# Kernel optimization log

Hardware: AMD Instinct MI355X
Metric: run time of the kernel (lower is better)

## Reference

```python
import jax, jax.numpy as jnp
import numpy as np

B, L, H = 2, 4096, 1024
ED, N, R, K = 2048, 16, 64, 4


def setup_inputs() -> dict:
    key = jax.random.key(0)
    ks = jax.random.split(key, 8)
    w = lambda i, shape, s=0.02: jax.random.normal(ks[i], shape, jnp.float32) * s
    # dt bias initialized like Mamba: inv-softplus of dt ~ logU(1e-3, 1e-1)
    dt = jnp.exp(jax.random.uniform(ks[7], (ED,)) * (np.log(0.1) - np.log(0.001)) + np.log(0.001))
    dt = jnp.clip(dt, 1e-4)
    inv_dt = dt + jnp.log(-jnp.expm1(-dt))
    A = jnp.broadcast_to(jnp.arange(1, N + 1, dtype=jnp.float32), (ED, N))
    return dict(
        x=jax.random.normal(ks[0], (B, L, H), jnp.float32),
        in_proj_w=w(1, (2 * ED, H)),
        conv_w=w(2, (ED, K), 0.2),
        conv_b=jnp.zeros((ED,), jnp.float32),
        x_proj_w=w(3, (R + 2 * N, ED)),
        dt_w=w(4, (ED, R), 64 ** -0.5),
        dt_b=inv_dt,
        A_log=jnp.log(A),
        D=jnp.ones((ED,), jnp.float32),
        out_proj_w=w(5, (H, ED)),
    )


def reference(x, in_proj_w, conv_w, conv_b, x_proj_w, dt_w, dt_b, A_log, D, out_proj_w):
    Bq, Lq, Hq = x.shape
    EDq, Kq = conv_w.shape
    Rq = dt_w.shape[1]
    Nq = A_log.shape[1]

    # in_proj -> [B, L, 2*ED]; chunk into hidden_states and gate
    xz = jnp.einsum('blh,eh->ble', x, in_proj_w)
    hs, gate = jnp.split(xz, 2, axis=-1)

    # causal depthwise conv1d along L (padding K-1 on the left), then SiLU
    hs_pad = jnp.pad(hs, ((0, 0), (Kq - 1, 0), (0, 0)))  # [B, L+K-1, ED]
    conv = conv_b
    for k in range(Kq):  # K=4, fixed small loop
        conv = conv + hs_pad[:, k:k + Lq, :] * conv_w[:, k]
    hs = jax.nn.silu(conv)  # [B, L, ED]

    # x_proj -> split into dt (rank R), B (N), C (N)
    ssm = jnp.einsum('ble,pe->blp', hs, x_proj_w)
    dtr, Bm, Cm = jnp.split(ssm, [Rq, Rq + Nq], axis=-1)

    # dt_proj + softplus (delta_softplus=True with delta_bias)
    delta = jax.nn.softplus(jnp.einsum('blr,er->ble', dtr, dt_w) + dt_b)  # [B,L,ED]

    A = -jnp.exp(A_log)  # [ED, N]

    # selective scan: h_t = exp(delta_t*A)*h_{t-1} + delta_t*B_t*u_t ; y_t = <h_t, C_t>
    def step(h, inp):
        d_t, B_t, C_t, u_t = inp  # [B,ED], [B,N], [B,N], [B,ED]
        dA = jnp.exp(d_t[..., None] * A)                      # [B,ED,N]
        h = dA * h + (d_t * u_t)[..., None] * B_t[:, None, :]  # [B,ED,N]
        y = jnp.einsum('ben,bn->be', h, C_t)                   # [B,ED]
        return h, y

    h0 = jnp.zeros((Bq, EDq, Nq), x.dtype)
    xs = (jnp.moveaxis(delta, 1, 0), jnp.moveaxis(Bm, 1, 0),
          jnp.moveaxis(Cm, 1, 0), jnp.moveaxis(hs, 1, 0))
    _, ys = jax.lax.scan(step, h0, xs)  # ys: [L, B, ED]

    y = jnp.moveaxis(ys, 0, 1) + hs * D      # skip term D*u
    y = y * jax.nn.silu(gate)                # gated output
    return jnp.einsum('ble,he->blh', y, out_proj_w)
```

## Files before the change

kernel.cpp:

```cpp
#include <hip/hip_runtime.h>


typedef float f32x4 __attribute__((ext_vector_type(4)));
typedef short short8 __attribute__((ext_vector_type(8)));

#define DEV __device__ __forceinline__

DEV float bf2f(unsigned short u) {
  union { unsigned int i; float f; } v; v.i = ((unsigned int)u) << 16; return v.f;
}
DEV unsigned short f2bf(float f) {
  union { float f; unsigned int i; } v; v.f = f;
  return (unsigned short)((v.i + 0x7fffu + ((v.i >> 16) & 1u)) >> 16);
}

DEV void gload_lds16(const void* g, void* l) {
  __builtin_amdgcn_global_load_lds(
      (const __attribute__((address_space(1))) unsigned int*)g,
      (__attribute__((address_space(3))) unsigned int*)l, 16, 0, 0);
}

DEV void mfma_bf16(f32x4& d, short8 a, short8 b) {
  asm("v_mfma_f32_16x16x32_bf16 %0, %1, %2, %0" : "+v"(d) : "v"(a), "v"(b));
}

template <int N> DEV void wait_vmcnt() {
  static_assert(N == 0 || N == 1 || N == 2 || N == 4 || N == 8, "unsupported");
  if constexpr (N == 0)      asm volatile("s_waitcnt vmcnt(0)" ::: "memory");
  else if constexpr (N == 1) asm volatile("s_waitcnt vmcnt(1)" ::: "memory");
  else if constexpr (N == 2) asm volatile("s_waitcnt vmcnt(2)" ::: "memory");
  else if constexpr (N == 4) asm volatile("s_waitcnt vmcnt(4)" ::: "memory");
  else                       asm volatile("s_waitcnt vmcnt(8)" ::: "memory");
}

template <int BM, int BN, int WM, int WN, int EPI>
__global__ __launch_bounds__(256) void gemm_bt_kernel(
    const unsigned short* __restrict__ A, const unsigned short* __restrict__ Bw,
    int M, int N, int Kd,
    float* __restrict__ o_f32, unsigned short* __restrict__ o_b16a,
    unsigned short* __restrict__ o_b16b, const float* __restrict__ bias,
    float* __restrict__ oB, float* __restrict__ oC)
{
  constexpr int MFR = BM / WM / 16;
  constexpr int NFR = BN / WN / 16;
  constexpr int TA = BM * 4;
  constexpr int TB = BN * 4;
  constexpr int TILE = (BM + BN) * 32;
  constexpr int LA3 = (TA > 192) ? ((TA - 193) / 256 + 1) : 0;
  constexpr int LB3 = (TB > 192) ? ((TB - 193) / 256 + 1) : 0;
  constexpr int LPS = LA3 + LB3;
  __shared__ unsigned short lds[TILE * 3];

  const int tid  = threadIdx.x;
  const int wave = tid >> 6;
  const int lane = tid & 63;
  const int row  = lane & 15;
  const int g    = lane >> 4;
  const int swz  = g ^ ((row >> 1) & 3);
  const int rowBase = blockIdx.y * BM;
  const int colBase = blockIdx.x * BN;
  const int WROW = (wave / WN) * (BM / WM);
  const int WCOL = (wave % WN) * (BN / WN);

  auto stage = [&](int kt, int bufbase) {
    const int kk = kt * 32;
#pragma unroll
    for (int c0 = 0; c0 < TA; c0 += 256) {
      int ch = c0 + tid;
      if (ch < TA) {
        int r = ch >> 2;
        int gs = (ch & 3) ^ ((r >> 1) & 3);
        gload_lds16(A + (size_t)(rowBase + r) * Kd + kk + gs * 8,
                    (void*)(lds + bufbase + (c0 + wave * 64) * 8));
      }
    }
#pragma unroll
    for (int c0 = 0; c0 < TB; c0 += 256) {
      int ch = c0 + tid;
      if (ch < TB) {
        int r = ch >> 2;
        int gs = (ch & 3) ^ ((r >> 1) & 3);
        gload_lds16(Bw + (size_t)(colBase + r) * Kd + kk + gs * 8,
                    (void*)(lds + bufbase + BM * 32 + (c0 + wave * 64) * 8));
      }
    }
  };

  f32x4 acc[MFR][NFR];
  const f32x4 fz = {0.f, 0.f, 0.f, 0.f};
#pragma unroll
  for (int i = 0; i < MFR; ++i)
#pragma unroll
    for (int j = 0; j < NFR; ++j) acc[i][j] = fz;

  const int nt = Kd / 32;
  stage(0, 0);
  stage(1, TILE);
  int cur = 0;
  for (int t = 0; t < nt; ++t) {
    if (t + 2 < nt) {
      int b2 = cur + 2; if (b2 >= 3) b2 -= 3;
      stage(t + 2, b2 * TILE);
      wait_vmcnt<2 * LPS>();
    } else if (t + 1 < nt) {
      wait_vmcnt<LPS>();
    } else {
      wait_vmcnt<0>();
    }
    __builtin_amdgcn_sched_barrier(0);
    __builtin_amdgcn_s_barrier();
    __builtin_amdgcn_sched_barrier(0);
    const unsigned short* lb = lds + cur * TILE;
    short8 af[MFR], bfr[NFR];
#pragma unroll
    for (int mi = 0; mi < MFR; ++mi)
      af[mi] = *(const short8*)(lb + (WROW + mi * 16 + row) * 32 + swz * 8);
#pragma unroll
    for (int ni = 0; ni < NFR; ++ni)
      bfr[ni] = *(const short8*)(lb + BM * 32 + (WCOL + ni * 16 + row) * 32 + swz * 8);
#pragma unroll
    for (int mi = 0; mi < MFR; ++mi)
#pragma unroll
      for (int ni = 0; ni < NFR; ++ni)
        mfma_bf16(acc[mi][ni], af[mi], bfr[ni]);
    __builtin_amdgcn_sched_barrier(0);
    __builtin_amdgcn_s_barrier();
    cur += 1; if (cur >= 3) cur -= 3;
  }

#pragma unroll
  for (int mi = 0; mi < MFR; ++mi) {
#pragma unroll
    for (int ni = 0; ni < NFR; ++ni) {
      const int gcol = colBase + WCOL + ni * 16 + row;
#pragma unroll
      for (int r = 0; r < 4; ++r) {
        const int grow = rowBase + WROW + mi * 16 + g * 4 + r;
        float v = acc[mi][ni][r];
        if constexpr (EPI == 0) {
          o_f32[(size_t)grow * N + gcol] = v;
        } else if constexpr (EPI == 1) {
          if (gcol < 2048) o_b16a[(size_t)grow * 2048 + gcol] = f2bf(v);
          else             o_b16b[(size_t)grow * 2048 + (gcol - 2048)] = f2bf(v);
        } else if constexpr (EPI == 2) {
          if (gcol < 64)      o_b16a[(size_t)grow * 64 + gcol] = f2bf(v);
          else if (gcol < 80) oB[(size_t)grow * 16 + (gcol - 64)] = v;
          else                oC[(size_t)grow * 16 + (gcol - 80)] = v;
        } else {
          float x = v + bias[gcol];
          o_f32[(size_t)grow * N + gcol] = (x > 20.f) ? x : __logf(1.f + __expf(x));
        }
      }
    }
  }
}

__global__ __launch_bounds__(256) void cvt_bf16_kernel(
    const float* __restrict__ in, unsigned short* __restrict__ out, int n8)
{
  int i = blockIdx.x * 256 + threadIdx.x;
  if (i >= n8) return;
  const float4* p = (const float4*)(in + (size_t)i * 8);
  float4 a = p[0], b = p[1];
  float v[8] = {a.x, a.y, a.z, a.w, b.x, b.y, b.z, b.w};
  unsigned o[4];
#pragma unroll
  for (int q = 0; q < 4; ++q)
    o[q] = (unsigned)f2bf(v[2 * q]) | ((unsigned)f2bf(v[2 * q + 1]) << 16);
  *(uint4*)(out + (size_t)i * 8) = make_uint4(o[0], o[1], o[2], o[3]);
}

__global__ __launch_bounds__(256) void conv_silu_kernel(
    const unsigned short* __restrict__ hsraw, const float* __restrict__ cw,
    const float* __restrict__ cb, unsigned short* __restrict__ hsb)
{
  int idx = blockIdx.x * 256 + threadIdx.x;
  int e0 = (idx & 255) * 8;
  int t  = (idx >> 8) & 4095;
  int b  = idx >> 20;
  float acc[8];
  float wv[4][8];
#pragma unroll
  for (int j = 0; j < 8; ++j) acc[j] = cb[e0 + j];
#pragma unroll
  for (int k = 0; k < 4; ++k)
#pragma unroll
    for (int j = 0; j < 8; ++j) wv[k][j] = cw[(e0 + j) * 4 + k];
#pragma unroll
  for (int k = 0; k < 4; ++k) {
    int tt = t - 3 + k;
    if (tt < 0) continue;
    uint4 v4 = *(const uint4*)(hsraw + ((size_t)(b * 4096 + tt)) * 2048 + e0);
    unsigned arr[4] = {v4.x, v4.y, v4.z, v4.w};
#pragma unroll
    for (int q = 0; q < 4; ++q) {
      acc[2 * q]     += wv[k][2 * q]     * bf2f((unsigned short)(arr[q] & 0xffffu));
      acc[2 * q + 1] += wv[k][2 * q + 1] * bf2f((unsigned short)(arr[q] >> 16));
    }
  }
  unsigned o[4];
#pragma unroll
  for (int q = 0; q < 4; ++q) {
    float a0 = acc[2 * q], a1 = acc[2 * q + 1];
    a0 = a0 / (1.f + __expf(-a0));
    a1 = a1 / (1.f + __expf(-a1));
    o[q] = (unsigned)f2bf(a0) | ((unsigned)f2bf(a1) << 16);
  }
  *(uint4*)(hsb + ((size_t)(b * 4096 + t)) * 2048 + e0) = make_uint4(o[0], o[1], o[2], o[3]);
}

__global__ __launch_bounds__(256) void scan_phase1(
    const float* __restrict__ delta, const unsigned short* __restrict__ hsb,
    const float* __restrict__ Bb, const float* __restrict__ alog,
    float* __restrict__ h_end, float* __restrict__ Ssum)
{
  __shared__ __align__(16) float Bs[64 * 16];
  const int tid = threadIdx.x;
  const int e = blockIdx.x * 256 + tid;
  const int c = blockIdx.y;
  const int b = blockIdx.z;
  const int t0 = c * 64;
  {
    const float* src = Bb + ((size_t)(b * 4096 + t0)) * 16;
#pragma unroll
    for (int k = 0; k < 4; ++k) Bs[tid + k * 256] = src[tid + k * 256];
  }
  float An[16];
  {
    const float4* ap = (const float4*)(alog + e * 16);
#pragma unroll
    for (int q = 0; q < 4; ++q) {
      float4 v = ap[q];
      An[4*q+0] = -__expf(v.x); An[4*q+1] = -__expf(v.y);
      An[4*q+2] = -__expf(v.z); An[4*q+3] = -__expf(v.w);
    }
  }
  __syncthreads();
  float h[16];
#pragma unroll
  for (int n = 0; n < 16; ++n) h[n] = 0.f;
  float sumd = 0.f;
  size_t base = ((size_t)(b * 4096 + t0)) * 2048 + e;
  float dd = delta[base];
  float uu = bf2f(hsb[base]);
  for (int j = 0; j < 64; ++j) {
    int jn = (j < 63) ? j + 1 : 63;
    float d_nxt = delta[base + (size_t)jn * 2048];
    float u_nxt = bf2f(hsb[base + (size_t)jn * 2048]);
    const float4* Bv = (const float4*)(Bs + j * 16);
    float4 b0 = Bv[0], b1 = Bv[1], b2 = Bv[2], b3 = Bv[3];
    float Bl[16] = {b0.x,b0.y,b0.z,b0.w, b1.x,b1.y,b1.z,b1.w,
                    b2.x,b2.y,b2.z,b2.w, b3.x,b3.y,b3.z,b3.w};
    sumd += dd;
    float du = dd * uu;
#pragma unroll
    for (int n = 0; n < 16; ++n)
      h[n] = fmaf(__expf(An[n] * dd), h[n], du * Bl[n]);
    dd = d_nxt; uu = u_nxt;
  }
  float* he = h_end + (((size_t)(b * 2048 + e)) * 64 + c) * 16;
#pragma unroll
  for (int q = 0; q < 4; ++q) {
    float4 v = {h[4*q], h[4*q+1], h[4*q+2], h[4*q+3]};
    *(float4*)(he + 4 * q) = v;
  }
  Ssum[((size_t)(b * 2048 + e)) * 64 + c] = sumd;
}

__global__ __launch_bounds__(256) void scan_phase2(
    const float* __restrict__ h_end, const float* __restrict__ Ssum,
    const float* __restrict__ alog, float* __restrict__ h_start)
{
  const int tid = threadIdx.x;
  const int n = tid & 15;
  const int G = blockIdx.x * 16 + (tid >> 4);
  const int e = G & 2047;
  const float An = -__expf(alog[e * 16 + n]);
  size_t hb = (size_t)G * 64 * 16 + n;
  size_t sb = (size_t)G * 64;
  float h = 0.f;
  constexpr int PF = 8;
  float hq[PF], Sq[PF];
#pragma unroll
  for (int j = 0; j < PF; ++j) { hq[j] = h_end[hb + (size_t)j * 16]; Sq[j] = Ssum[sb + j]; }
  for (int c0 = 0; c0 < 64; c0 += PF) {
    float hn[PF], Sn[PF];
#pragma unroll
    for (int j = 0; j < PF; ++j) {
      int cn = c0 + PF + j; cn = (cn < 64) ? cn : 63;
      hn[j] = h_end[hb + (size_t)cn * 16]; Sn[j] = Ssum[sb + cn];
    }
#pragma unroll
    for (int j = 0; j < PF; ++j) {
      h_start[hb + (size_t)(c0 + j) * 16] = h;
      h = fmaf(__expf(An * Sq[j]), h, hq[j]);
    }
#pragma unroll
    for (int j = 0; j < PF; ++j) { hq[j] = hn[j]; Sq[j] = Sn[j]; }
  }
}

__global__ __launch_bounds__(256) void scan_phase3(
    const float* __restrict__ delta, const unsigned short* __restrict__ hsb,
    const float* __restrict__ Bb, const float* __restrict__ Cb,
    const float* __restrict__ alog, const float* __restrict__ h_start,
    const float* __restrict__ Dv, unsigned short* __restrict__ gate_y2)
{
  __shared__ __align__(16) float Bs[64 * 16];
  __shared__ __align__(16) float Cs[64 * 16];
  const int tid = threadIdx.x;
  const int e = blockIdx.x * 256 + tid;
  const int c = blockIdx.y;
  const int b = blockIdx.z;
  const int t0 = c * 64;
  {
    const float* srcB = Bb + ((size_t)(b * 4096 + t0)) * 16;
    const float* srcC = Cb + ((size_t)(b * 4096 + t0)) * 16;
#pragma unroll
    for (int k = 0; k < 4; ++k) {
      Bs[tid + k * 256] = srcB[tid + k * 256];
      Cs[tid + k * 256] = srcC[tid + k * 256];
    }
  }
  float An[16];
  {
    const float4* ap = (const float4*)(alog + e * 16);
#pragma unroll
    for (int q = 0; q < 4; ++q) {
      float4 v = ap[q];
      An[4*q+0] = -__expf(v.x); An[4*q+1] = -__expf(v.y);
      An[4*q+2] = -__expf(v.z); An[4*q+3] = -__expf(v.w);
    }
  }
  const float De = Dv[e];
  float h[16];
  {
    const float4* hp = (const float4*)(h_start + (((size_t)(b * 2048 + e)) * 64 + c) * 16);
#pragma unroll
    for (int q = 0; q < 4; ++q) {
      float4 v = hp[q];
      h[4*q+0] = v.x; h[4*q+1] = v.y; h[4*q+2] = v.z; h[4*q+3] = v.w;
    }
  }
  __syncthreads();
  size_t base = ((size_t)(b * 4096 + t0)) * 2048 + e;
  float dd = delta[base];
  float uu = bf2f(hsb[base]);
  float gg = bf2f(gate_y2[base]);
  for (int j = 0; j < 64; ++j) {
    int jn = (j < 63) ? j + 1 : 63;
    float d_nxt = delta[base + (size_t)jn * 2048];
    float u_nxt = bf2f(hsb[base + (size_t)jn * 2048]);
    float g_nxt = bf2f(gate_y2[base + (size_t)jn * 2048]);
    const float4* Bv = (const float4*)(Bs + j * 16);
    const float4* Cv = (const float4*)(Cs + j * 16);
    float4 b0 = Bv[0], b1 = Bv[1], b2 = Bv[2], b3 = Bv[3];
    float4 c0v = Cv[0], c1v = Cv[1], c2v = Cv[2], c3v = Cv[3];
    float Bl[16] = {b0.x,b0.y,b0.z,b0.w, b1.x,b1.y,b1.z,b1.w,
                    b2.x,b2.y,b2.z,b2.w, b3.x,b3.y,b3.z,b3.w};
    float Cl[16] = {c0v.x,c0v.y,c0v.z,c0v.w, c1v.x,c1v.y,c1v.z,c1v.w,
                    c2v.x,c2v.y,c2v.z,c2v.w, c3v.x,c3v.y,c3v.z,c3v.w};
    float du = dd * uu;
    float y = 0.f;
#pragma unroll
    for (int n = 0; n < 16; ++n) {
      h[n] = fmaf(__expf(An[n] * dd), h[n], du * Bl[n]);
      y = fmaf(h[n], Cl[n], y);
    }
    float val = (y + uu * De) * (gg / (1.f + __expf(-gg)));
    gate_y2[base + (size_t)j * 2048] = f2bf(val);
    dd = d_nxt; uu = u_nxt; gg = g_nxt;
  }
}

extern "C" void kernel_launch(void* const* d_in, const int* in_sizes, int n_in,
                              void* d_out, int out_size, void* d_ws, size_t ws_size,
                              hipStream_t stream)
{
  const float* x    = (const float*)d_in[0];
  const float* w1   = (const float*)d_in[1];
  const float* cw   = (const float*)d_in[2];
  const float* cb   = (const float*)d_in[3];
  const float* xp   = (const float*)d_in[4];
  const float* dtw  = (const float*)d_in[5];
  const float* dtb  = (const float*)d_in[6];
  const float* alog = (const float*)d_in[7];
  const float* Dp   = (const float*)d_in[8];
  const float* wo   = (const float*)d_in[9];
  float* out = (float*)d_out;
  char* ws = (char*)d_ws;

  const size_t o_xb    = 0;
  const size_t o_wb1   = 16777216;
  const size_t o_xpb   = 25165824;
  const size_t o_dtwb  = 25559040;
  const size_t o_wob   = 25821184;
  const size_t o_hsraw = 30015488;
  const size_t o_gate  = 63569920;
  const size_t o_hsb   = 97124352;
  const size_t o_dtrb  = 130678784;
  const size_t o_Bb    = 131727360;
  const size_t o_Cb    = 132251648;
  const size_t o_delta = 132775936;
  const size_t WS_NEED = o_delta + 67108864 + 262144;
  if (ws_size < WS_NEED) return;

  unsigned short* xb    = (unsigned short*)(ws + o_xb);
  unsigned short* wb1   = (unsigned short*)(ws + o_wb1);
  unsigned short* xpb   = (unsigned short*)(ws + o_xpb);
  unsigned short* dtwb  = (unsigned short*)(ws + o_dtwb);
  unsigned short* wob   = (unsigned short*)(ws + o_wob);
  unsigned short* hsraw = (unsigned short*)(ws + o_hsraw);
  unsigned short* gate  = (unsigned short*)(ws + o_gate);
  unsigned short* hsb   = (unsigned short*)(ws + o_hsb);
  unsigned short* dtrb  = (unsigned short*)(ws + o_dtrb);
  float* Bb    = (float*)(ws + o_Bb);
  float* Cb    = (float*)(ws + o_Cb);
  float* delta = (float*)(ws + o_delta);
  float* h_end   = (float*)(ws + o_xb);
  float* h_start = (float*)(ws + o_hsraw);
  float* Ssum    = (float*)(ws + o_hsraw + 16777216);

  cvt_bf16_kernel<<<4096, 256, 0, stream>>>(x,   xb,   1048576);
  cvt_bf16_kernel<<<2048, 256, 0, stream>>>(w1,  wb1,  524288);
  cvt_bf16_kernel<<<96,   256, 0, stream>>>(xp,  xpb,  24576);
  cvt_bf16_kernel<<<64,   256, 0, stream>>>(dtw, dtwb, 16384);
  cvt_bf16_kernel<<<1024, 256, 0, stream>>>(wo,  wob,  262144);

  gemm_bt_kernel<128,128,2,2,1><<<dim3(32,64), 256, 0, stream>>>(
      xb, wb1, 8192, 4096, 1024, nullptr, hsraw, gate, nullptr, nullptr, nullptr);
  conv_silu_kernel<<<8192, 256, 0, stream>>>(hsraw, cw, cb, hsb);
  gemm_bt_kernel<32,96,2,2,2><<<dim3(1,256), 256, 0, stream>>>(
      hsb, xpb, 8192, 96, 2048, nullptr, dtrb, nullptr, nullptr, Bb, Cb);
  gemm_bt_kernel<64,64,2,2,3><<<dim3(32,128), 256, 0, stream>>>(
      dtrb, dtwb, 8192, 2048, 64, delta, nullptr, nullptr, dtb, nullptr, nullptr);

  scan_phase1<<<dim3(8, 64, 2), 256, 0, stream>>>(delta, hsb, Bb, alog, h_end, Ssum);
  scan_phase2<<<256, 256, 0, stream>>>(h_end, Ssum, alog, h_start);
  scan_phase3<<<dim3(8, 64, 2), 256, 0, stream>>>(
      delta, hsb, Bb, Cb, alog, h_start, Dp, gate);

  gemm_bt_kernel<128,128,2,2,0><<<dim3(8,64), 256, 0, stream>>>(
      gate, wob, 8192, 1024, 2048, out, nullptr, nullptr, nullptr, nullptr, nullptr);
}
```

Baseline: 386.1 us.

## Use 256x256-tile 8-wave pipelined GEMM for in_proj

Adds a new GEMM kernel with 256x256 output tiles, 512 threads, K-step 64 and double-buffered LDS. LDS reads are interleaved with MFMA quadrants and paired with barriers and s_setprio. Workgroup indices are swizzled across XCD groups. Only the in_proj GEMM (8192x4096x1024) switches to it, aiming for more data reuse per load and better overlap of loads with compute. The cost is 128KB of LDS per block, heavy register pressure from 128 accumulator floats per lane, and many barriers.

```diff
diff --git a/kernel.cpp b/kernel.cpp
--- a/kernel.cpp
+++ b/kernel.cpp
@@ -3,15 +3,16 @@
 
 typedef float f32x4 __attribute__((ext_vector_type(4)));
 typedef short short8 __attribute__((ext_vector_type(8)));
+typedef unsigned short u16;
 
 #define DEV __device__ __forceinline__
 
-DEV float bf2f(unsigned short u) {
+DEV float bf2f(u16 u) {
   union { unsigned int i; float f; } v; v.i = ((unsigned int)u) << 16; return v.f;
 }
-DEV unsigned short f2bf(float f) {
+DEV u16 f2bf(float f) {
   union { float f; unsigned int i; } v; v.f = f;
-  return (unsigned short)((v.i + 0x7fffu + ((v.i >> 16) & 1u)) >> 16);
+  return (u16)((v.i + 0x7fffu + ((v.i >> 16) & 1u)) >> 16);
 }
 
 DEV void gload_lds16(const void* g, void* l) {
@@ -25,20 +26,150 @@
 }
 
 template <int N> DEV void wait_vmcnt() {
-  static_assert(N == 0 || N == 1 || N == 2 || N == 4 || N == 8, "unsupported");
   if constexpr (N == 0)      asm volatile("s_waitcnt vmcnt(0)" ::: "memory");
   else if constexpr (N == 1) asm volatile("s_waitcnt vmcnt(1)" ::: "memory");
   else if constexpr (N == 2) asm volatile("s_waitcnt vmcnt(2)" ::: "memory");
   else if constexpr (N == 4) asm volatile("s_waitcnt vmcnt(4)" ::: "memory");
+  else if constexpr (N == 6) asm volatile("s_waitcnt vmcnt(6)" ::: "memory");
   else                       asm volatile("s_waitcnt vmcnt(8)" ::: "memory");
+}
+
+#define SYNC_PRE() do { __builtin_amdgcn_s_barrier(); \
+  asm volatile("s_waitcnt lgkmcnt(0)" ::: "memory"); \
+  __builtin_amdgcn_sched_barrier(0); \
+  __builtin_amdgcn_s_setprio(1); } while (0)
+#define SYNC_POST() do { __builtin_amdgcn_s_setprio(0); \
+  __builtin_amdgcn_sched_barrier(0); \
+  __builtin_amdgcn_s_barrier(); } while (0)
+
+template <int EPI>
+__global__ __launch_bounds__(512, 2) void gemm256_kernel(
+    const u16* __restrict__ A, const u16* __restrict__ Bw,
+    int M, int N, int Kd,
+    float* __restrict__ o_f32, u16* __restrict__ o_b16a, u16* __restrict__ o_b16b)
+{
+  __shared__ u16 lds[65536];
+  const int tid  = threadIdx.x;
+  const int wave = tid >> 6;
+  const int lane = tid & 63;
+  const int row  = lane & 15;
+  const int g    = lane >> 4;
+  const int wr   = wave >> 2;
+  const int wc   = wave & 3;
+
+  const int nbx = N >> 8;
+  const int nwg = gridDim.x;
+  const int cpx = nwg >> 3;
+  const int swzb = (blockIdx.x & 7) * cpx + (blockIdx.x >> 3);
+  const int bx = swzb % nbx, by = swzb / nbx;
+  const int rowBase = by * 256, colBase = bx * 256;
+
+  auto STAGE = [&](int isB, int h, int kt) {
+    const u16* src = isB ? Bw : A;
+    const int baseRow = (isB ? colBase : rowBase) + h * 128;
+    const int ldsbase = (kt & 1) * 32768 + isB * 16384 + h * 8192;
+    const int kk = kt * 64;
+#pragma unroll
+    for (int q = 0; q < 2; ++q) {
+      int c = q * 512 + tid;
+      int r = c >> 3;
+      int qc = (c & 7) ^ (r & 7);
+      gload_lds16(src + (size_t)(baseRow + r) * Kd + kk + qc * 8,
+                  (void*)(lds + ldsbase + (q * 512 + wave * 64) * 8));
+    }
+  };
+
+  f32x4 acc[8][4];
+#pragma unroll
+  for (int i = 0; i < 8; ++i)
+#pragma unroll
+    for (int j = 0; j < 4; ++j) acc[i][j] = (f32x4){0.f, 0.f, 0.f, 0.f};
+
+  short8 rA[8], rB0[4], rB1[4];
+
+#define LDA(PAR, MH) do { \
+  _Pragma("unroll") for (int mi = 0; mi < 4; ++mi) \
+  _Pragma("unroll") for (int ks = 0; ks < 2; ++ks) \
+    rA[mi*2+ks] = *(const short8*)(lds + (PAR)*32768 + wr*8192 \
+        + ((MH)*64 + mi*16 + row)*64 + (((ks*4 + g) ^ (row & 7))*8)); \
+} while (0)
+
+#define LDB(PAR, NH, RB) do { \
+  _Pragma("unroll") for (int ni = 0; ni < 2; ++ni) \
+  _Pragma("unroll") for (int ks = 0; ks < 2; ++ks) \
+    (RB)[ni*2+ks] = *(const short8*)(lds + (PAR)*32768 + 16384 + (wc>>1)*8192 \
+        + (((wc&1)*64 + (NH)*32 + ni*16 + row)*64) + (((ks*4 + g) ^ (row & 7))*8)); \
+} while (0)
+
+#define QUAD(MH, NH, RB) do { \
+  _Pragma("unroll") for (int mi = 0; mi < 4; ++mi) \
+  _Pragma("unroll") for (int ni = 0; ni < 2; ++ni) \
+  _Pragma("unroll") for (int ks = 0; ks < 2; ++ks) \
+    mfma_bf16(acc[(MH)*4+mi][(NH)*2+ni], rA[mi*2+ks], (RB)[ni*2+ks]); \
+} while (0)
+
+  const int nkt = Kd >> 6;
+  const int niters = nkt >> 1;
+
+  STAGE(0, 0, 0); STAGE(0, 1, 0); STAGE(1, 0, 0); STAGE(1, 1, 0);
+  STAGE(1, 0, 1); STAGE(1, 1, 1); STAGE(0, 0, 1);
+  wait_vmcnt<6>();
+  __builtin_amdgcn_s_barrier();
+
+  for (int i = 0; i < niters; ++i) {
+    const int kt0 = 2 * i, kt1 = 2 * i + 1;
+    const bool pf = (i + 1 < niters);
+    LDA(0, 0); LDB(0, 0, rB0); STAGE(0, 1, kt1);
+    SYNC_PRE(); QUAD(0, 0, rB0); SYNC_POST();
+    LDB(0, 1, rB1);
+    SYNC_PRE(); QUAD(0, 1, rB1); SYNC_POST();
+    LDA(0, 1);
+    if (pf) { STAGE(1, 0, kt0 + 2); STAGE(1, 1, kt0 + 2); }
+    SYNC_PRE(); QUAD(1, 0, rB0); SYNC_POST();
+    if (pf) { STAGE(0, 0, kt0 + 2); wait_vmcnt<6>(); } else { wait_vmcnt<0>(); }
+    SYNC_PRE(); QUAD(1, 1, rB1); SYNC_POST();
+    LDA(1, 0); LDB(1, 0, rB0);
+    if (pf) STAGE(0, 1, kt0 + 2);
+    SYNC_PRE(); QUAD(0, 0, rB0); SYNC_POST();
+    LDB(1, 1, rB1);
+    SYNC_PRE(); QUAD(0, 1, rB1); SYNC_POST();
+    LDA(1, 1);
+    if (pf) { STAGE(1, 0, kt1 + 2); STAGE(1, 1, kt1 + 2); }
+    SYNC_PRE(); QUAD(1, 0, rB0); SYNC_POST();
+    if (pf) { STAGE(0, 0, kt1 + 2); wait_vmcnt<6>(); } else { wait_vmcnt<0>(); }
+    SYNC_PRE(); QUAD(1, 1, rB1); SYNC_POST();
+  }
+#undef LDA
+#undef LDB
+#undef QUAD
+
+#pragma unroll
+  for (int mf = 0; mf < 8; ++mf) {
+    const int growb = rowBase + wr * 128 + (mf >> 2) * 64 + (mf & 3) * 16 + g * 4;
+#pragma unroll
+    for (int nf = 0; nf < 4; ++nf) {
+      const int gcol = colBase + wc * 64 + (nf >> 1) * 32 + (nf & 1) * 16 + row;
+#pragma unroll
+      for (int r4 = 0; r4 < 4; ++r4) {
+        const int grow = growb + r4;
+        float v = acc[mf][nf][r4];
+        if constexpr (EPI == 0) {
+          o_f32[(size_t)grow * N + gcol] = v;
+        } else {
+          if (gcol < 2048) o_b16a[(size_t)grow * 2048 + gcol] = f2bf(v);
+          else             o_b16b[(size_t)grow * 2048 + (gcol - 2048)] = f2bf(v);
+        }
+      }
+    }
+  }
 }
 
 template <int BM, int BN, int WM, int WN, int EPI>
 __global__ __launch_bounds__(256) void gemm_bt_kernel(
-    const unsigned short* __restrict__ A, const unsigned short* __restrict__ Bw,
+    const u16* __restrict__ A, const u16* __restrict__ Bw,
     int M, int N, int Kd,
-    float* __restrict__ o_f32, unsigned short* __restrict__ o_b16a,
-    unsigned short* __restrict__ o_b16b, const float* __restrict__ bias,
+    float* __restrict__ o_f32, u16* __restrict__ o_b16a,
+    u16* __restrict__ o_b16b, const float* __restrict__ bias,
     float* __restrict__ oB, float* __restrict__ oC)
 {
   constexpr int MFR = BM / WM / 16;
@@ -49,7 +180,7 @@
   constexpr int LA3 = (TA > 192) ? ((TA - 193) / 256 + 1) : 0;
   constexpr int LB3 = (TB > 192) ? ((TB - 193) / 256 + 1) : 0;
   constexpr int LPS = LA3 + LB3;
-  __shared__ unsigned short lds[TILE * 3];
+  __shared__ u16 lds[TILE * 3];
 
   const int tid  = threadIdx.x;
   const int wave = tid >> 6;
@@ -87,11 +218,10 @@
   };
 
   f32x4 acc[MFR][NFR];
-  const f32x4 fz = {0.f, 0.f, 0.f, 0.f};
 #pragma unroll
   for (int i = 0; i < MFR; ++i)
 #pragma unroll
-    for (int j = 0; j < NFR; ++j) acc[i][j] = fz;
+    for (int j = 0; j < NFR; ++j) acc[i][j] = (f32x4){0.f, 0.f, 0.f, 0.f};
 
   const int nt = Kd / 32;
   stage(0, 0);
@@ -110,7 +240,7 @@
     __builtin_amdgcn_sched_barrier(0);
     __builtin_amdgcn_s_barrier();
     __builtin_amdgcn_sched_barrier(0);
-    const unsigned short* lb = lds + cur * TILE;
+    const u16* lb = lds + cur * TILE;
     short8 af[MFR], bfr[NFR];
 #pragma unroll
     for (int mi = 0; mi < MFR; ++mi)
@@ -156,7 +286,7 @@
 }
 
 __global__ __launch_bounds__(256) void cvt_bf16_kernel(
-    const float* __restrict__ in, unsigned short* __restrict__ out, int n8)
+    const float* __restrict__ in, u16* __restrict__ out, int n8)
 {
   int i = blockIdx.x * 256 + threadIdx.x;
   if (i >= n8) return;
@@ -171,8 +301,8 @@
 }
 
 __global__ __launch_bounds__(256) void conv_silu_kernel(
-    const unsigned short* __restrict__ hsraw, const float* __restrict__ cw,
-    const float* __restrict__ cb, unsigned short* __restrict__ hsb)
+    const u16* __restrict__ hsraw, const float* __restrict__ cw,
+    const float* __restrict__ cb, u16* __restrict__ hsb)
 {
   int idx = blockIdx.x * 256 + threadIdx.x;
   int e0 = (idx & 255) * 8;
@@ -194,8 +324,8 @@
     unsigned arr[4] = {v4.x, v4.y, v4.z, v4.w};
 #pragma unroll
     for (int q = 0; q < 4; ++q) {
-      acc[2 * q]     += wv[k][2 * q]     * bf2f((unsigned short)(arr[q] & 0xffffu));
-      acc[2 * q + 1] += wv[k][2 * q + 1] * bf2f((unsigned short)(arr[q] >> 16));
+      acc[2 * q]     += wv[k][2 * q]     * bf2f((u16)(arr[q] & 0xffffu));
+      acc[2 * q + 1] += wv[k][2 * q + 1] * bf2f((u16)(arr[q] >> 16));
     }
   }
   unsigned o[4];
@@ -210,7 +340,7 @@
 }
 
 __global__ __launch_bounds__(256) void scan_phase1(
-    const float* __restrict__ delta, const unsigned short* __restrict__ hsb,
+    const float* __restrict__ delta, const u16* __restrict__ hsb,
     const float* __restrict__ Bb, const float* __restrict__ alog,
     float* __restrict__ h_end, float* __restrict__ Ssum)
 {
@@ -301,10 +431,10 @@
 }
 
 __global__ __launch_bounds__(256) void scan_phase3(
-    const float* __restrict__ delta, const unsigned short* __restrict__ hsb,
+    const float* __restrict__ delta, const u16* __restrict__ hsb,
     const float* __restrict__ Bb, const float* __restrict__ Cb,
     const float* __restrict__ alog, const float* __restrict__ h_start,
-    const float* __restrict__ Dv, unsigned short* __restrict__ gate_y2)
+    const float* __restrict__ Dv, u16* __restrict__ gate_y2)
 {
   __shared__ __align__(16) float Bs[64 * 16];
   __shared__ __align__(16) float Cs[64 * 16];
@@ -405,15 +535,15 @@
   const size_t WS_NEED = o_delta + 67108864 + 262144;
   if (ws_size < WS_NEED) return;
 
-  unsigned short* xb    = (unsigned short*)(ws + o_xb);
-  unsigned short* wb1   = (unsigned short*)(ws + o_wb1);
-  unsigned short* xpb   = (unsigned short*)(ws + o_xpb);
-  unsigned short* dtwb  = (unsigned short*)(ws + o_dtwb);
-  unsigned short* wob   = (unsigned short*)(ws + o_wob);
-  unsigned short* hsraw = (unsigned short*)(ws + o_hsraw);
-  unsigned short* gate  = (unsigned short*)(ws + o_gate);
-  unsigned short* hsb   = (unsigned short*)(ws + o_hsb);
-  unsigned short* dtrb  = (unsigned short*)(ws + o_dtrb);
+  u16* xb    = (u16*)(ws + o_xb);
+  u16* wb1   = (u16*)(ws + o_wb1);
+  u16* xpb   = (u16*)(ws + o_xpb);
+  u16* dtwb  = (u16*)(ws + o_dtwb);
+  u16* wob   = (u16*)(ws + o_wob);
+  u16* hsraw = (u16*)(ws + o_hsraw);
+  u16* gate  = (u16*)(ws + o_gate);
+  u16* hsb   = (u16*)(ws + o_hsb);
+  u16* dtrb  = (u16*)(ws + o_dtrb);
   float* Bb    = (float*)(ws + o_Bb);
   float* Cb    = (float*)(ws + o_Cb);
   float* delta = (float*)(ws + o_delta);
@@ -427,8 +557,8 @@
   cvt_bf16_kernel<<<64,   256, 0, stream>>>(dtw, dtwb, 16384);
   cvt_bf16_kernel<<<1024, 256, 0, stream>>>(wo,  wob,  262144);
 
-  gemm_bt_kernel<128,128,2,2,1><<<dim3(32,64), 256, 0, stream>>>(
-      xb, wb1, 8192, 4096, 1024, nullptr, hsraw, gate, nullptr, nullptr, nullptr);
+  gemm256_kernel<1><<<512, 512, 0, stream>>>(
+      xb, wb1, 8192, 4096, 1024, nullptr, hsraw, gate);
   conv_silu_kernel<<<8192, 256, 0, stream>>>(hsraw, cw, cb, hsb);
   gemm_bt_kernel<32,96,2,2,2><<<dim3(1,256), 256, 0, stream>>>(
       hsb, xpb, 8192, 96, 2048, nullptr, dtrb, nullptr, nullptr, Bb, Cb);
```

Result: faster. 376.5 us (-2.5%).
